# Kernel optimization log

Hardware: AMD Instinct MI355X
Metric: run time of the kernel (lower is better)

Reference implementation:

```python
import jax, jax.numpy as jnp
import numpy as np

B, T, N, H, P = 16, 64, 512, 128, 12


def _laplacian_with_self_loop(adj):
    a = adj + jnp.eye(adj.shape[0], dtype=adj.dtype)
    d_inv_sqrt = 1.0 / jnp.sqrt(a.sum(axis=1))
    return a * d_inv_sqrt[:, None] * d_inv_sqrt[None, :]


def setup_inputs() -> dict:
    key = jax.random.key(0)
    ks = jax.random.split(key, 10)
    inputs = jax.random.normal(ks[0], (B, T, N), dtype=jnp.float32)
    adj = jax.random.uniform(ks[1], (N, N), dtype=jnp.float32)
    adj = (adj + adj.T) * 0.5
    laplacian = _laplacian_with_self_loop(adj)

    def xavier(k, shape):
        fan_in, fan_out = shape[0], shape[1]
        lim = np.sqrt(6.0 / (fan_in + fan_out))
        return jax.random.uniform(k, shape, jnp.float32, -lim, lim)

    W1 = xavier(ks[2], (H + 1, 2 * H))      # graph_conv1 weights
    b1 = jnp.ones((2 * H,), jnp.float32)    # bias init 1.0
    W2 = xavier(ks[3], (H + 1, H))          # graph_conv2 weights
    b2 = jnp.zeros((H,), jnp.float32)
    att_w1 = xavier(ks[4], (H, 1))
    att_w2 = xavier(ks[5], (N, 1))
    att_w3 = xavier(ks[6], (N, 1))
    att_b1 = jnp.zeros((1,), jnp.float32)
    att_b2 = jnp.zeros((1,), jnp.float32)
    att_b3 = jnp.zeros((1,), jnp.float32)
    W_out = xavier(ks[7], (T, P))
    b_out = jnp.zeros((P,), jnp.float32)
    return dict(inputs=inputs, laplacian=laplacian, W1=W1, b1=b1, W2=W2, b2=b2,
                att_w1=att_w1, att_w2=att_w2, att_w3=att_w3,
                att_b1=att_b1, att_b2=att_b2, att_b3=att_b3,
                W_out=W_out, b_out=b_out)


def reference(inputs, laplacian, W1, b1, W2, b2,
              att_w1, att_w2, att_w3, att_b1, att_b2, att_b3,
              W_out, b_out):
    Bs, Ts, Ns = inputs.shape
    Hs = W2.shape[1]

    def graph_conv(x_t, h_flat, W, b):
        # x_t: [B,N]; h_flat: [B, N*H]
        h = h_flat.reshape(Bs, Ns, Hs)
        conc = jnp.concatenate([x_t[..., None], h], axis=-1)     # [B,N,H+1]
        agg = jnp.einsum('mn,bnc->bmc', laplacian, conc)          # [B,N,H+1]
        out = agg @ W + b                                         # [B,N,O]
        return out.reshape(Bs, -1)                                # [B,N*O] (flattened, matching torch)

    def step(h_flat, x_t):
        ru = jax.nn.sigmoid(graph_conv(x_t, h_flat, W1, b1))      # [B, N*2H]
        r, u = jnp.split(ru, 2, axis=1)                            # split on flattened dim (faithful)
        c = jnp.tanh(graph_conv(x_t, r * h_flat, W2, b2))          # [B, N*H]
        new_h = u * h_flat + (1.0 - u) * c
        return new_h, new_h

    h0 = jnp.zeros((Bs, Ns * Hs), inputs.dtype)
    _, hs = jax.lax.scan(step, h0, jnp.moveaxis(inputs, 1, 0))     # [T,B,N*H]
    hidden_states = jnp.moveaxis(hs, 0, 1).reshape(Bs, Ts, Ns, Hs)

    # SelfAttention: project H->1, then N->1 per (b,t), softmax over T
    hs1 = hidden_states.reshape(-1, Hs) @ att_w1 + att_b1          # [B*T*N, 1]
    f = (hs1.reshape(-1, Ns) @ att_w2 + att_b2).reshape(Bs, Ts)
    g = (hs1.reshape(-1, Ns) @ att_w3 + att_b3).reshape(Bs, Ts)
    beta = jax.nn.softmax(g * f, axis=-1)                          # [B,T]
    context = beta[:, :, None] * hs1.reshape(Bs, Ts, Ns)           # [B,T,N]

    context = context.transpose(0, 2, 1)                           # [B,N,T]
    Ps = W_out.shape[1]
    out = (context.reshape(-1, Ts) @ W_out + b_out).reshape(Bs, Ns, Ps)
    return out.transpose(0, 2, 1)                                  # [B,pre_len,N]
```

## Files before the change

kernel.cpp:

```cpp
#include <hip/hip_runtime.h>
#include <math.h>

#define B_ 16
#define T_ 64
#define N_ 512
#define H_ 128
#define P_ 12
#define NH 65536

__global__ __launch_bounds__(512) void lx_kernel(const float* __restrict__ x,
                                                 const float* __restrict__ L,
                                                 float* __restrict__ Lx) {
    __shared__ __align__(16) float xs[4][N_];
    const int r0 = blockIdx.x * 4;
    const int tid = threadIdx.x;
    for (int j = 0; j < 4; ++j)
        xs[j][tid] = x[(size_t)(r0 + j) * N_ + tid];
    __syncthreads();
    float a0 = 0.f, a1 = 0.f, a2 = 0.f, a3 = 0.f;
    const int m = tid;
#pragma unroll 8
    for (int n = 0; n < N_; ++n) {
        float lv = L[(size_t)n * N_ + m];
        a0 += xs[0][n] * lv;
        a1 += xs[1][n] * lv;
        a2 += xs[2][n] * lv;
        a3 += xs[3][n] * lv;
    }
    Lx[(size_t)(r0 + 0) * N_ + m] = a0;
    Lx[(size_t)(r0 + 1) * N_ + m] = a1;
    Lx[(size_t)(r0 + 2) * N_ + m] = a2;
    Lx[(size_t)(r0 + 3) * N_ + m] = a3;
}

__global__ __launch_bounds__(512) void gc1_kernel(
    const float* __restrict__ L, const float* __restrict__ Hprev,
    const float* __restrict__ Lx, const float* __restrict__ W1,
    const float* __restrict__ b1, float* __restrict__ rh,
    float* __restrict__ u, int t) {
    union Sm {
        struct { float Ht[2][64][128]; float Lt[2][64][33]; } p;
        float Wt[32][260];
    };
    __shared__ __align__(16) Sm sm;
    __shared__ __align__(16) float Zs[4][32][128];

    const int tid = threadIdx.x;
    const int b = blockIdx.x & 15;
    const int m0 = (blockIdx.x >> 4) * 32;
    const int g = tid >> 7;
    const int gt = tid & 127;
    const int tx = gt & 31, ty = gt >> 5;
    const int c0 = tx * 4;

    const float* __restrict__ Hb = Hprev + (size_t)b * NH;

    const int hrow = tid >> 5, hcol = (tid & 31) * 4;
    const int lm = tid >> 4, lk0 = (tid & 15) * 4;

    {
#pragma unroll
        for (int jj = 0; jj < 4; ++jj)
            *(float4*)&sm.p.Ht[0][hrow + 16 * jj][hcol] =
                *(const float4*)&Hb[(size_t)(hrow + 16 * jj) * H_ + hcol];
        float4 lv = *(const float4*)&L[(size_t)(m0 + lm) * N_ + lk0];
        sm.p.Lt[0][lk0 + 0][lm] = lv.x;
        sm.p.Lt[0][lk0 + 1][lm] = lv.y;
        sm.p.Lt[0][lk0 + 2][lm] = lv.z;
        sm.p.Lt[0][lk0 + 3][lm] = lv.w;
    }
    __syncthreads();

    float acc[8][4] = {};

    for (int kc = 0; kc < 8; ++kc) {
        const int bi = kc & 1, bj = bi ^ 1;
        float4 h0, h1, h2, h3, lv;
        if (kc < 7) {
            const size_t kb2 = (size_t)(kc + 1) * 64;
            h0 = *(const float4*)&Hb[(kb2 + hrow) * H_ + hcol];
            h1 = *(const float4*)&Hb[(kb2 + hrow + 16) * H_ + hcol];
            h2 = *(const float4*)&Hb[(kb2 + hrow + 32) * H_ + hcol];
            h3 = *(const float4*)&Hb[(kb2 + hrow + 48) * H_ + hcol];
            lv = *(const float4*)&L[(size_t)(m0 + lm) * N_ + kb2 + lk0];
        }
#pragma unroll
        for (int kk = 0; kk < 16; ++kk) {
            const int k = g * 16 + kk;
            const float4 la = *(const float4*)&sm.p.Lt[bi][k][ty * 8];
            const float4 lb = *(const float4*)&sm.p.Lt[bi][k][ty * 8 + 4];
            const float4 hv = *(const float4*)&sm.p.Ht[bi][k][c0];
#define FMA_ROW(r, s)                                                   \
            acc[r][0] += (s) * hv.x; acc[r][1] += (s) * hv.y;           \
            acc[r][2] += (s) * hv.z; acc[r][3] += (s) * hv.w;
            FMA_ROW(0, la.x) FMA_ROW(1, la.y) FMA_ROW(2, la.z) FMA_ROW(3, la.w)
            FMA_ROW(4, lb.x) FMA_ROW(5, lb.y) FMA_ROW(6, lb.z) FMA_ROW(7, lb.w)
#undef FMA_ROW
        }
        if (kc < 7) {
            *(float4*)&sm.p.Ht[bj][hrow][hcol] = h0;
            *(float4*)&sm.p.Ht[bj][hrow + 16][hcol] = h1;
            *(float4*)&sm.p.Ht[bj][hrow + 32][hcol] = h2;
            *(float4*)&sm.p.Ht[bj][hrow + 48][hcol] = h3;
            sm.p.Lt[bj][lk0 + 0][lm] = lv.x;
            sm.p.Lt[bj][lk0 + 1][lm] = lv.y;
            sm.p.Lt[bj][lk0 + 2][lm] = lv.z;
            sm.p.Lt[bj][lk0 + 3][lm] = lv.w;
        }
        __syncthreads();
    }

#pragma unroll
    for (int r = 0; r < 8; ++r)
        *(float4*)&Zs[g][ty * 8 + r][c0] =
            make_float4(acc[r][0], acc[r][1], acc[r][2], acc[r][3]);
    __syncthreads();

    for (int j = tid; j < 1024; j += 512) {
        const int m = j >> 5, cc = (j & 31) * 4;
        float4 z0 = *(const float4*)&Zs[0][m][cc];
        float4 z1 = *(const float4*)&Zs[1][m][cc];
        float4 z2 = *(const float4*)&Zs[2][m][cc];
        float4 z3 = *(const float4*)&Zs[3][m][cc];
        *(float4*)&Zs[0][m][cc] = make_float4(z0.x + z1.x + z2.x + z3.x,
                                              z0.y + z1.y + z2.y + z3.y,
                                              z0.z + z1.z + z2.z + z3.z,
                                              z0.w + z1.w + z2.w + z3.w);
    }
    __syncthreads();

    const int to = tid & 63, tm = tid >> 6;
    const int o0 = to * 4;
    float a2[4][4] = {};
    const int wr = tid >> 4, wc = (tid & 15) * 16;

    for (int c4 = 0; c4 < 4; ++c4) {
#pragma unroll
        for (int jj = 0; jj < 4; ++jj)
            *(float4*)&sm.Wt[wr][wc + 4 * jj] =
                *(const float4*)&W1[(size_t)(1 + c4 * 32 + wr) * 256 + wc + 4 * jj];
        __syncthreads();
#pragma unroll
        for (int ch4 = 0; ch4 < 8; ++ch4) {
            const float4 w0v = *(const float4*)&sm.Wt[ch4 * 4 + 0][o0];
            const float4 w1v = *(const float4*)&sm.Wt[ch4 * 4 + 1][o0];
            const float4 w2v = *(const float4*)&sm.Wt[ch4 * 4 + 2][o0];
            const float4 w3v = *(const float4*)&sm.Wt[ch4 * 4 + 3][o0];
#pragma unroll
            for (int i = 0; i < 4; ++i) {
                const float4 zv = *(const float4*)&Zs[0][tm + 8 * i][c4 * 32 + ch4 * 4];
                a2[i][0] += zv.x * w0v.x + zv.y * w1v.x + zv.z * w2v.x + zv.w * w3v.x;
                a2[i][1] += zv.x * w0v.y + zv.y * w1v.y + zv.z * w2v.y + zv.w * w3v.y;
                a2[i][2] += zv.x * w0v.z + zv.y * w1v.z + zv.z * w2v.z + zv.w * w3v.z;
                a2[i][3] += zv.x * w0v.w + zv.y * w1v.w + zv.z * w2v.w + zv.w * w3v.w;
            }
        }
        __syncthreads();
    }

    const float4 w0r = *(const float4*)&W1[o0];
    const float4 bbv = *(const float4*)&b1[o0];
    const float* __restrict__ LxRow = Lx + ((size_t)b * T_ + t) * N_ + m0;
    float* __restrict__ rhB = rh + (size_t)b * NH;
    float* __restrict__ uB = u + (size_t)b * NH;
    const bool isR = (m0 < 256);
#pragma unroll
    for (int i = 0; i < 4; ++i) {
        const int mi = tm + 8 * i;
        const float lx = LxRow[mi];
        float v0 = a2[i][0] + lx * w0r.x + bbv.x;
        float v1 = a2[i][1] + lx * w0r.y + bbv.y;
        float v2 = a2[i][2] + lx * w0r.z + bbv.z;
        float v3 = a2[i][3] + lx * w0r.w + bbv.w;
        float s0 = 1.f / (1.f + expf(-v0));
        float s1 = 1.f / (1.f + expf(-v1));
        float s2 = 1.f / (1.f + expf(-v2));
        float s3 = 1.f / (1.f + expf(-v3));
        const int fl = (m0 + mi) * 256 + o0;
        if (isR) {
            float4 hv = *(const float4*)&Hb[fl];
            *(float4*)&rhB[fl] = make_float4(s0 * hv.x, s1 * hv.y, s2 * hv.z, s3 * hv.w);
        } else {
            *(float4*)&uB[fl - NH] = make_float4(s0, s1, s2, s3);
        }
    }
}

__global__ __launch_bounds__(512) void gc2_kernel(
    const float* __restrict__ L, const float* __restrict__ Hprev,
    const float* __restrict__ rh, const float* __restrict__ u,
    const float* __restrict__ Lx, const float* __restrict__ W2,
    const float* __restrict__ b2, const float* __restrict__ aw1,
    const float* __restrict__ ab1, float* __restrict__ Hnew,
    float* __restrict__ hs1, int t) {
    union Sm {
        struct { float Ht[2][64][128]; float Lt[2][64][33]; } p;
        float Wt[32][132];
    };
    __shared__ __align__(16) Sm sm;
    __shared__ __align__(16) float Zs[4][32][128];
    __shared__ __align__(16) float red[32][32];

    const int tid = threadIdx.x;
    const int b = blockIdx.x & 15;
    const int m0 = (blockIdx.x >> 4) * 32;
    const int g = tid >> 7;
    const int gt = tid & 127;
    const int tx = gt & 31, ty = gt >> 5;
    const int c0 = tx * 4;

    const float* __restrict__ Rb = rh + (size_t)b * NH;
    const float* __restrict__ Hb = Hprev + (size_t)b * NH;
    const float* __restrict__ Ub = u + (size_t)b * NH;

    const int hrow = tid >> 5, hcol = (tid & 31) * 4;
    const int lm = tid >> 4, lk0 = (tid & 15) * 4;

    {
#pragma unroll
        for (int jj = 0; jj < 4; ++jj)
            *(float4*)&sm.p.Ht[0][hrow + 16 * jj][hcol] =
                *(const float4*)&Rb[(size_t)(hrow + 16 * jj) * H_ + hcol];
        float4 lv = *(const float4*)&L[(size_t)(m0 + lm) * N_ + lk0];
        sm.p.Lt[0][lk0 + 0][lm] = lv.x;
        sm.p.Lt[0][lk0 + 1][lm] = lv.y;
        sm.p.Lt[0][lk0 + 2][lm] = lv.z;
        sm.p.Lt[0][lk0 + 3][lm] = lv.w;
    }
    __syncthreads();

    float acc[8][4] = {};

    for (int kc = 0; kc < 8; ++kc) {
        const int bi = kc & 1, bj = bi ^ 1;
        float4 h0, h1, h2, h3, lv;
        if (kc < 7) {
            const size_t kb2 = (size_t)(kc + 1) * 64;
            h0 = *(const float4*)&Rb[(kb2 + hrow) * H_ + hcol];
            h1 = *(const float4*)&Rb[(kb2 + hrow + 16) * H_ + hcol];
            h2 = *(const float4*)&Rb[(kb2 + hrow + 32) * H_ + hcol];
            h3 = *(const float4*)&Rb[(kb2 + hrow + 48) * H_ + hcol];
            lv = *(const float4*)&L[(size_t)(m0 + lm) * N_ + kb2 + lk0];
        }
#pragma unroll
        for (int kk = 0; kk < 16; ++kk) {
            const int k = g * 16 + kk;
            const float4 la = *(const float4*)&sm.p.Lt[bi][k][ty * 8];
            const float4 lb = *(const float4*)&sm.p.Lt[bi][k][ty * 8 + 4];
            const float4 hv = *(const float4*)&sm.p.Ht[bi][k][c0];
#define FMA_ROW(r, s)                                                   \
            acc[r][0] += (s) * hv.x; acc[r][1] += (s) * hv.y;           \
            acc[r][2] += (s) * hv.z; acc[r][3] += (s) * hv.w;
            FMA_ROW(0, la.x) FMA_ROW(1, la.y) FMA_ROW(2, la.z) FMA_ROW(3, la.w)
            FMA_ROW(4, lb.x) FMA_ROW(5, lb.y) FMA_ROW(6, lb.z) FMA_ROW(7, lb.w)
#undef FMA_ROW
        }
        if (kc < 7) {
            *(float4*)&sm.p.Ht[bj][hrow][hcol] = h0;
            *(float4*)&sm.p.Ht[bj][hrow + 16][hcol] = h1;
            *(float4*)&sm.p.Ht[bj][hrow + 32][hcol] = h2;
            *(float4*)&sm.p.Ht[bj][hrow + 48][hcol] = h3;
            sm.p.Lt[bj][lk0 + 0][lm] = lv.x;
            sm.p.Lt[bj][lk0 + 1][lm] = lv.y;
            sm.p.Lt[bj][lk0 + 2][lm] = lv.z;
            sm.p.Lt[bj][lk0 + 3][lm] = lv.w;
        }
        __syncthreads();
    }

#pragma unroll
    for (int r = 0; r < 8; ++r)
        *(float4*)&Zs[g][ty * 8 + r][c0] =
            make_float4(acc[r][0], acc[r][1], acc[r][2], acc[r][3]);
    __syncthreads();

    for (int j = tid; j < 1024; j += 512) {
        const int m = j >> 5, cc = (j & 31) * 4;
        float4 z0 = *(const float4*)&Zs[0][m][cc];
        float4 z1 = *(const float4*)&Zs[1][m][cc];
        float4 z2 = *(const float4*)&Zs[2][m][cc];
        float4 z3 = *(const float4*)&Zs[3][m][cc];
        *(float4*)&Zs[0][m][cc] = make_float4(z0.x + z1.x + z2.x + z3.x,
                                              z0.y + z1.y + z2.y + z3.y,
                                              z0.z + z1.z + z2.z + z3.z,
                                              z0.w + z1.w + z2.w + z3.w);
    }
    __syncthreads();

    const int to = tid & 31, tm = tid >> 5;
    const int o0 = to * 4;
    float a2[2][4] = {};
    const int wr = tid >> 4, wc = (tid & 15) * 8;

    for (int c4 = 0; c4 < 4; ++c4) {
#pragma unroll
        for (int jj = 0; jj < 2; ++jj)
            *(float4*)&sm.Wt[wr][wc + 4 * jj] =
                *(const float4*)&W2[(size_t)(1 + c4 * 32 + wr) * H_ + wc + 4 * jj];
        __syncthreads();
#pragma unroll
        for (int ch4 = 0; ch4 < 8; ++ch4) {
            const float4 w0v = *(const float4*)&sm.Wt[ch4 * 4 + 0][o0];
            const float4 w1v = *(const float4*)&sm.Wt[ch4 * 4 + 1][o0];
            const float4 w2v = *(const float4*)&sm.Wt[ch4 * 4 + 2][o0];
            const float4 w3v = *(const float4*)&sm.Wt[ch4 * 4 + 3][o0];
#pragma unroll
            for (int i = 0; i < 2; ++i) {
                const float4 zv = *(const float4*)&Zs[0][tm + 16 * i][c4 * 32 + ch4 * 4];
                a2[i][0] += zv.x * w0v.x + zv.y * w1v.x + zv.z * w2v.x + zv.w * w3v.x;
                a2[i][1] += zv.x * w0v.y + zv.y * w1v.y + zv.z * w2v.y + zv.w * w3v.y;
                a2[i][2] += zv.x * w0v.z + zv.y * w1v.z + zv.z * w2v.z + zv.w * w3v.z;
                a2[i][3] += zv.x * w0v.w + zv.y * w1v.w + zv.z * w2v.w + zv.w * w3v.w;
            }
        }
        __syncthreads();
    }

    const float4 w0r = *(const float4*)&W2[o0];
    const float4 bbv = *(const float4*)&b2[o0];
    const float4 awv = *(const float4*)&aw1[o0];
    const float* __restrict__ LxRow = Lx + ((size_t)b * T_ + t) * N_ + m0;
    float* __restrict__ HnB = Hnew + (size_t)b * NH;
#pragma unroll
    for (int i = 0; i < 2; ++i) {
        const int mi = tm + 16 * i;
        const float lx = LxRow[mi];
        float c0e = tanhf(a2[i][0] + lx * w0r.x + bbv.x);
        float c1e = tanhf(a2[i][1] + lx * w0r.y + bbv.y);
        float c2e = tanhf(a2[i][2] + lx * w0r.z + bbv.z);
        float c3e = tanhf(a2[i][3] + lx * w0r.w + bbv.w);
        const int fl = (m0 + mi) * H_ + o0;
        float4 uv = *(const float4*)&Ub[fl];
        float4 hp = *(const float4*)&Hb[fl];
        float h0 = uv.x * hp.x + (1.f - uv.x) * c0e;
        float h1 = uv.y * hp.y + (1.f - uv.y) * c1e;
        float h2 = uv.z * hp.z + (1.f - uv.z) * c2e;
        float h3 = uv.w * hp.w + (1.f - uv.w) * c3e;
        *(float4*)&HnB[fl] = make_float4(h0, h1, h2, h3);
        red[mi][to] = h0 * awv.x + h1 * awv.y + h2 * awv.z + h3 * awv.w;
    }
    __syncthreads();
    if (tid < 32) {
        float s = 0.f;
#pragma unroll
        for (int k2 = 0; k2 < 32; ++k2) s += red[tid][k2];
        hs1[((size_t)b * T_ + t) * N_ + m0 + tid] = s + ab1[0];
    }
}

__global__ __launch_bounds__(64) void att_beta_kernel(
    const float* __restrict__ hs1, const float* __restrict__ aw2,
    const float* __restrict__ aw3, const float* __restrict__ ab2,
    const float* __restrict__ ab3, float* __restrict__ beta) {
    const int b = blockIdx.x;
    const int t = threadIdx.x;
    const float* __restrict__ row = hs1 + ((size_t)b * T_ + t) * N_;
    float f = 0.f, g = 0.f;
    for (int n = 0; n < N_; n += 4) {
        float4 hv = *(const float4*)&row[n];
        float4 w2v = *(const float4*)&aw2[n];
        float4 w3v = *(const float4*)&aw3[n];
        f += hv.x * w2v.x + hv.y * w2v.y + hv.z * w2v.z + hv.w * w2v.w;
        g += hv.x * w3v.x + hv.y * w3v.y + hv.z * w3v.z + hv.w * w3v.w;
    }
    f += ab2[0];
    g += ab3[0];
    float s = f * g;
    float mx = s;
    for (int off = 32; off; off >>= 1) mx = fmaxf(mx, __shfl_xor(mx, off));
    float e = expf(s - mx);
    float sum = e;
    for (int off = 32; off; off >>= 1) sum += __shfl_xor(sum, off);
    beta[b * T_ + t] = e / sum;
}

__global__ __launch_bounds__(256) void att_out_kernel(
    const float* __restrict__ hs1, const float* __restrict__ beta,
    const float* __restrict__ Wout, const float* __restrict__ bout,
    float* __restrict__ out) {
    __shared__ float bs[T_];
    __shared__ float ws[T_][P_];
    const int b = blockIdx.x;
    const int tid = threadIdx.x;
    if (tid < T_) bs[tid] = beta[b * T_ + tid];
    for (int i = tid; i < T_ * P_; i += 256) ws[i / P_][i % P_] = Wout[i];
    __syncthreads();
    for (int nn = 0; nn < 2; ++nn) {
        const int n = tid + nn * 256;
        float acc[P_];
#pragma unroll
        for (int p = 0; p < P_; ++p) acc[p] = bout[p];
        for (int t = 0; t < T_; ++t) {
            float v = bs[t] * hs1[((size_t)b * T_ + t) * N_ + n];
#pragma unroll
            for (int p = 0; p < P_; ++p) acc[p] += v * ws[t][p];
        }
#pragma unroll
        for (int p = 0; p < P_; ++p) out[((size_t)b * P_ + p) * N_ + n] = acc[p];
    }
}

extern "C" void kernel_launch(void* const* d_in, const int* in_sizes, int n_in,
                              void* d_out, int out_size, void* d_ws, size_t ws_size,
                              hipStream_t stream) {
    const float* x = (const float*)d_in[0];
    const float* L = (const float*)d_in[1];
    const float* W1 = (const float*)d_in[2];
    const float* b1 = (const float*)d_in[3];
    const float* W2 = (const float*)d_in[4];
    const float* b2 = (const float*)d_in[5];
    const float* aw1 = (const float*)d_in[6];
    const float* aw2 = (const float*)d_in[7];
    const float* aw3 = (const float*)d_in[8];
    const float* ab1 = (const float*)d_in[9];
    const float* ab2 = (const float*)d_in[10];
    const float* ab3 = (const float*)d_in[11];
    const float* Wout = (const float*)d_in[12];
    const float* bout = (const float*)d_in[13];
    float* out = (float*)d_out;

    float* ws = (float*)d_ws;
    float* Lx = ws;
    float* hs1 = Lx + B_ * T_ * N_;
    float* hb0 = hs1 + B_ * T_ * N_;
    float* hb1 = hb0 + (size_t)B_ * NH;
    float* rh = hb1 + (size_t)B_ * NH;
    float* u = rh + (size_t)B_ * NH;
    float* beta = u + (size_t)B_ * NH;
    (void)in_sizes; (void)n_in; (void)out_size; (void)ws_size;

    hipMemsetAsync(hb0, 0, (size_t)B_ * NH * sizeof(float), stream);
    lx_kernel<<<256, 512, 0, stream>>>(x, L, Lx);

    for (int t = 0; t < T_; ++t) {
        float* hp = (t & 1) ? hb1 : hb0;
        float* hn = (t & 1) ? hb0 : hb1;
        gc1_kernel<<<256, 512, 0, stream>>>(L, hp, Lx, W1, b1, rh, u, t);
        gc2_kernel<<<256, 512, 0, stream>>>(L, hp, rh, u, Lx, W2, b2, aw1, ab1,
                                            hn, hs1, t);
    }
    att_beta_kernel<<<16, 64, 0, stream>>>(hs1, aw2, aw3, ab2, ab3, beta);
    att_out_kernel<<<16, 256, 0, stream>>>(hs1, beta, Wout, bout, out);
}
```

Measured before the change: 4.448 ms.

## Shrink graph-conv tiles and shared memory to raise occupancy

Both GRU graph-conv kernels move from 64-wide K chunks with 4-way split-K and 8x4 register tiles to 32-wide K chunks with 2-way split-K and 4x4 register tiles. The weight staging buffer is halved to 16 rows. Together this cuts shared memory (no 4x Zs reduction buffer) and per-thread registers, so more blocks can sit on each CU. The cost is twice as many barrier-separated iterations and less arithmetic per shared-memory load.

Measured after the change: 4.008 ms. 9.9% less time.

```diff
diff --git a/kernel.cpp b/kernel.cpp
--- a/kernel.cpp
+++ b/kernel.cpp
@@ -38,117 +38,110 @@
     const float* __restrict__ Lx, const float* __restrict__ W1,
     const float* __restrict__ b1, float* __restrict__ rh,
     float* __restrict__ u, int t) {
-    union Sm {
-        struct { float Ht[2][64][128]; float Lt[2][64][33]; } p;
-        float Wt[32][260];
+    __shared__ __align__(16) float Ht[2][32][H_];
+    union LW {
+        float Lt[2][32][33];
+        float Wt[16][260];
     };
-    __shared__ __align__(16) Sm sm;
-    __shared__ __align__(16) float Zs[4][32][128];
+    __shared__ __align__(16) LW sm;
+    __shared__ __align__(16) float Zb[32][H_];
 
     const int tid = threadIdx.x;
     const int b = blockIdx.x & 15;
     const int m0 = (blockIdx.x >> 4) * 32;
-    const int g = tid >> 7;
-    const int gt = tid & 127;
+    const float* __restrict__ Hb = Hprev + (size_t)b * NH;
+
+    const int hrow = tid >> 5, hcol = (tid & 31) * 4;
+    const int lm = tid >> 4, lk0 = (tid & 15) * 2;
+
+    {
+        *(float4*)&Ht[0][hrow][hcol] = *(const float4*)&Hb[(size_t)hrow * H_ + hcol];
+        *(float4*)&Ht[0][hrow + 16][hcol] =
+            *(const float4*)&Hb[(size_t)(hrow + 16) * H_ + hcol];
+        float2 lv = *(const float2*)&L[(size_t)(m0 + lm) * N_ + lk0];
+        sm.Lt[0][lk0 + 0][lm] = lv.x;
+        sm.Lt[0][lk0 + 1][lm] = lv.y;
+    }
+    __syncthreads();
+
+    const int g = tid >> 8;
+    const int gt = tid & 255;
     const int tx = gt & 31, ty = gt >> 5;
-    const int c0 = tx * 4;
-
-    const float* __restrict__ Hb = Hprev + (size_t)b * NH;
-
-    const int hrow = tid >> 5, hcol = (tid & 31) * 4;
-    const int lm = tid >> 4, lk0 = (tid & 15) * 4;
-
-    {
-#pragma unroll
-        for (int jj = 0; jj < 4; ++jj)
-            *(float4*)&sm.p.Ht[0][hrow + 16 * jj][hcol] =
-                *(const float4*)&Hb[(size_t)(hrow + 16 * jj) * H_ + hcol];
-        float4 lv = *(const float4*)&L[(size_t)(m0 + lm) * N_ + lk0];
-        sm.p.Lt[0][lk0 + 0][lm] = lv.x;
-        sm.p.Lt[0][lk0 + 1][lm] = lv.y;
-        sm.p.Lt[0][lk0 + 2][lm] = lv.z;
-        sm.p.Lt[0][lk0 + 3][lm] = lv.w;
-    }
-    __syncthreads();
-
-    float acc[8][4] = {};
-
-    for (int kc = 0; kc < 8; ++kc) {
+    const int c0 = tx * 4, mrow = ty * 4;
+
+    float acc[4][4] = {};
+
+    for (int kc = 0; kc < 16; ++kc) {
         const int bi = kc & 1, bj = bi ^ 1;
-        float4 h0, h1, h2, h3, lv;
-        if (kc < 7) {
-            const size_t kb2 = (size_t)(kc + 1) * 64;
-            h0 = *(const float4*)&Hb[(kb2 + hrow) * H_ + hcol];
-            h1 = *(const float4*)&Hb[(kb2 + hrow + 16) * H_ + hcol];
-            h2 = *(const float4*)&Hb[(kb2 + hrow + 32) * H_ + hcol];
-            h3 = *(const float4*)&Hb[(kb2 + hrow + 48) * H_ + hcol];
-            lv = *(const float4*)&L[(size_t)(m0 + lm) * N_ + kb2 + lk0];
+        float4 p0, p1;
+        float2 pl;
+        if (kc < 15) {
+            const size_t kb = (size_t)(kc + 1) * 32;
+            p0 = *(const float4*)&Hb[(kb + hrow) * H_ + hcol];
+            p1 = *(const float4*)&Hb[(kb + hrow + 16) * H_ + hcol];
+            pl = *(const float2*)&L[(size_t)(m0 + lm) * N_ + kb + lk0];
         }
 #pragma unroll
         for (int kk = 0; kk < 16; ++kk) {
             const int k = g * 16 + kk;
-            const float4 la = *(const float4*)&sm.p.Lt[bi][k][ty * 8];
-            const float4 lb = *(const float4*)&sm.p.Lt[bi][k][ty * 8 + 4];
-            const float4 hv = *(const float4*)&sm.p.Ht[bi][k][c0];
-#define FMA_ROW(r, s)                                                   \
-            acc[r][0] += (s) * hv.x; acc[r][1] += (s) * hv.y;           \
-            acc[r][2] += (s) * hv.z; acc[r][3] += (s) * hv.w;
-            FMA_ROW(0, la.x) FMA_ROW(1, la.y) FMA_ROW(2, la.z) FMA_ROW(3, la.w)
-            FMA_ROW(4, lb.x) FMA_ROW(5, lb.y) FMA_ROW(6, lb.z) FMA_ROW(7, lb.w)
-#undef FMA_ROW
-        }
-        if (kc < 7) {
-            *(float4*)&sm.p.Ht[bj][hrow][hcol] = h0;
-            *(float4*)&sm.p.Ht[bj][hrow + 16][hcol] = h1;
-            *(float4*)&sm.p.Ht[bj][hrow + 32][hcol] = h2;
-            *(float4*)&sm.p.Ht[bj][hrow + 48][hcol] = h3;
-            sm.p.Lt[bj][lk0 + 0][lm] = lv.x;
-            sm.p.Lt[bj][lk0 + 1][lm] = lv.y;
-            sm.p.Lt[bj][lk0 + 2][lm] = lv.z;
-            sm.p.Lt[bj][lk0 + 3][lm] = lv.w;
-        }
-        __syncthreads();
-    }
-
-#pragma unroll
-    for (int r = 0; r < 8; ++r)
-        *(float4*)&Zs[g][ty * 8 + r][c0] =
-            make_float4(acc[r][0], acc[r][1], acc[r][2], acc[r][3]);
-    __syncthreads();
-
-    for (int j = tid; j < 1024; j += 512) {
-        const int m = j >> 5, cc = (j & 31) * 4;
-        float4 z0 = *(const float4*)&Zs[0][m][cc];
-        float4 z1 = *(const float4*)&Zs[1][m][cc];
-        float4 z2 = *(const float4*)&Zs[2][m][cc];
-        float4 z3 = *(const float4*)&Zs[3][m][cc];
-        *(float4*)&Zs[0][m][cc] = make_float4(z0.x + z1.x + z2.x + z3.x,
-                                              z0.y + z1.y + z2.y + z3.y,
-                                              z0.z + z1.z + z2.z + z3.z,
-                                              z0.w + z1.w + z2.w + z3.w);
+            const float4 la = *(const float4*)&sm.Lt[bi][k][mrow];
+            const float4 hv = *(const float4*)&Ht[bi][k][c0];
+            acc[0][0] += la.x * hv.x; acc[0][1] += la.x * hv.y;
+            acc[0][2] += la.x * hv.z; acc[0][3] += la.x * hv.w;
+            acc[1][0] += la.y * hv.x; acc[1][1] += la.y * hv.y;
+            acc[1][2] += la.y * hv.z; acc[1][3] += la.y * hv.w;
+            acc[2][0] += la.z * hv.x; acc[2][1] += la.z * hv.y;
+            acc[2][2] += la.z * hv.z; acc[2][3] += la.z * hv.w;
+            acc[3][0] += la.w * hv.x; acc[3][1] += la.w * hv.y;
+            acc[3][2] += la.w * hv.z; acc[3][3] += la.w * hv.w;
+        }
+        if (kc < 15) {
+            *(float4*)&Ht[bj][hrow][hcol] = p0;
+            *(float4*)&Ht[bj][hrow + 16][hcol] = p1;
+            sm.Lt[bj][lk0 + 0][lm] = pl.x;
+            sm.Lt[bj][lk0 + 1][lm] = pl.y;
+        }
+        __syncthreads();
+    }
+
+    if (g == 1) {
+#pragma unroll
+        for (int i = 0; i < 4; ++i)
+            *(float4*)&Zb[mrow + i][c0] =
+                make_float4(acc[i][0], acc[i][1], acc[i][2], acc[i][3]);
+    }
+    __syncthreads();
+    if (g == 0) {
+#pragma unroll
+        for (int i = 0; i < 4; ++i) {
+            float4 z = *(const float4*)&Zb[mrow + i][c0];
+            *(float4*)&Zb[mrow + i][c0] = make_float4(
+                acc[i][0] + z.x, acc[i][1] + z.y, acc[i][2] + z.z, acc[i][3] + z.w);
+        }
     }
     __syncthreads();
 
     const int to = tid & 63, tm = tid >> 6;
     const int o0 = to * 4;
     float a2[4][4] = {};
-    const int wr = tid >> 4, wc = (tid & 15) * 16;
-
-    for (int c4 = 0; c4 < 4; ++c4) {
-#pragma unroll
-        for (int jj = 0; jj < 4; ++jj)
-            *(float4*)&sm.Wt[wr][wc + 4 * jj] =
-                *(const float4*)&W1[(size_t)(1 + c4 * 32 + wr) * 256 + wc + 4 * jj];
-        __syncthreads();
-#pragma unroll
-        for (int ch4 = 0; ch4 < 8; ++ch4) {
+    const int wr = tid >> 5, wc = (tid & 31) * 4;
+
+    for (int ck = 0; ck < 8; ++ck) {
+        *(float4*)&sm.Wt[wr][wc] =
+            *(const float4*)&W1[(size_t)(1 + ck * 16 + wr) * 256 + wc];
+        *(float4*)&sm.Wt[wr][wc + 128] =
+            *(const float4*)&W1[(size_t)(1 + ck * 16 + wr) * 256 + wc + 128];
+        __syncthreads();
+#pragma unroll
+        for (int ch4 = 0; ch4 < 4; ++ch4) {
             const float4 w0v = *(const float4*)&sm.Wt[ch4 * 4 + 0][o0];
             const float4 w1v = *(const float4*)&sm.Wt[ch4 * 4 + 1][o0];
             const float4 w2v = *(const float4*)&sm.Wt[ch4 * 4 + 2][o0];
             const float4 w3v = *(const float4*)&sm.Wt[ch4 * 4 + 3][o0];
+            const int cc = ck * 16 + ch4 * 4;
 #pragma unroll
             for (int i = 0; i < 4; ++i) {
-                const float4 zv = *(const float4*)&Zs[0][tm + 8 * i][c4 * 32 + ch4 * 4];
+                const float4 zv = *(const float4*)&Zb[tm + 8 * i][cc];
                 a2[i][0] += zv.x * w0v.x + zv.y * w1v.x + zv.z * w2v.x + zv.w * w3v.x;
                 a2[i][1] += zv.x * w0v.y + zv.y * w1v.y + zv.z * w2v.y + zv.w * w3v.y;
                 a2[i][2] += zv.x * w0v.z + zv.y * w1v.z + zv.z * w2v.z + zv.w * w3v.z;
@@ -193,120 +186,111 @@
     const float* __restrict__ b2, const float* __restrict__ aw1,
     const float* __restrict__ ab1, float* __restrict__ Hnew,
     float* __restrict__ hs1, int t) {
-    union Sm {
-        struct { float Ht[2][64][128]; float Lt[2][64][33]; } p;
-        float Wt[32][132];
+    __shared__ __align__(16) float Ht[2][32][H_];
+    union LW {
+        float Lt[2][32][33];
+        float Wt[16][132];
     };
-    __shared__ __align__(16) Sm sm;
-    __shared__ __align__(16) float Zs[4][32][128];
+    __shared__ __align__(16) LW sm;
+    __shared__ __align__(16) float Zb[32][H_];
     __shared__ __align__(16) float red[32][32];
 
     const int tid = threadIdx.x;
     const int b = blockIdx.x & 15;
     const int m0 = (blockIdx.x >> 4) * 32;
-    const int g = tid >> 7;
-    const int gt = tid & 127;
-    const int tx = gt & 31, ty = gt >> 5;
-    const int c0 = tx * 4;
-
     const float* __restrict__ Rb = rh + (size_t)b * NH;
     const float* __restrict__ Hb = Hprev + (size_t)b * NH;
     const float* __restrict__ Ub = u + (size_t)b * NH;
 
     const int hrow = tid >> 5, hcol = (tid & 31) * 4;
-    const int lm = tid >> 4, lk0 = (tid & 15) * 4;
+    const int lm = tid >> 4, lk0 = (tid & 15) * 2;
 
     {
-#pragma unroll
-        for (int jj = 0; jj < 4; ++jj)
-            *(float4*)&sm.p.Ht[0][hrow + 16 * jj][hcol] =
-                *(const float4*)&Rb[(size_t)(hrow + 16 * jj) * H_ + hcol];
-        float4 lv = *(const float4*)&L[(size_t)(m0 + lm) * N_ + lk0];
-        sm.p.Lt[0][lk0 + 0][lm] = lv.x;
-        sm.p.Lt[0][lk0 + 1][lm] = lv.y;
-        sm.p.Lt[0][lk0 + 2][lm] = lv.z;
-        sm.p.Lt[0][lk0 + 3][lm] = lv.w;
-    }
-    __syncthreads();
-
-    float acc[8][4] = {};
-
-    for (int kc = 0; kc < 8; ++kc) {
+        *(float4*)&Ht[0][hrow][hcol] = *(const float4*)&Rb[(size_t)hrow * H_ + hcol];
+        *(float4*)&Ht[0][hrow + 16][hcol] =
+            *(const float4*)&Rb[(size_t)(hrow + 16) * H_ + hcol];
+        float2 lv = *(const float2*)&L[(size_t)(m0 + lm) * N_ + lk0];
+        sm.Lt[0][lk0 + 0][lm] = lv.x;
+        sm.Lt[0][lk0 + 1][lm] = lv.y;
+    }
+    __syncthreads();
+
+    const int g = tid >> 8;
+    const int gt = tid & 255;
+    const int tx = gt & 31, ty = gt >> 5;
+    const int c0 = tx * 4, mrow = ty * 4;
+
+    float acc[4][4] = {};
+
+    for (int kc = 0; kc < 16; ++kc) {
         const int bi = kc & 1, bj = bi ^ 1;
-        float4 h0, h1, h2, h3, lv;
-        if (kc < 7) {
-            const size_t kb2 = (size_t)(kc + 1) * 64;
-            h0 = *(const float4*)&Rb[(kb2 + hrow) * H_ + hcol];
-            h1 = *(const float4*)&Rb[(kb2 + hrow + 16) * H_ + hcol];
-            h2 = *(const float4*)&Rb[(kb2 + hrow + 32) * H_ + hcol];
-            h3 = *(const float4*)&Rb[(kb2 + hrow + 48) * H_ + hcol];
-            lv = *(const float4*)&L[(size_t)(m0 + lm) * N_ + kb2 + lk0];
+        float4 p0, p1;
+        float2 pl;
+        if (kc < 15) {
+            const size_t kb = (size_t)(kc + 1) * 32;
+            p0 = *(const float4*)&Rb[(kb + hrow) * H_ + hcol];
+            p1 = *(const float4*)&Rb[(kb + hrow + 16) * H_ + hcol];
+            pl = *(const float2*)&L[(size_t)(m0 + lm) * N_ + kb + lk0];
         }
 #pragma unroll
         for (int kk = 0; kk < 16; ++kk) {
             const int k = g * 16 + kk;
-            const float4 la = *(const float4*)&sm.p.Lt[bi][k][ty * 8];
-            const float4 lb = *(const float4*)&sm.p.Lt[bi][k][ty * 8 + 4];
-            const float4 hv = *(const float4*)&sm.p.Ht[bi][k][c0];
-#define FMA_ROW(r, s)                                                   \
-            acc[r][0] += (s) * hv.x; acc[r][1] += (s) * hv.y;           \
-            acc[r][2] += (s) * hv.z; acc[r][3] += (s) * hv.w;
-            FMA_ROW(0, la.x) FMA_ROW(1, la.y) FMA_ROW(2, la.z) FMA_ROW(3, la.w)
-            FMA_ROW(4, lb.x) FMA_ROW(5, lb.y) FMA_ROW(6, lb.z) FMA_ROW(7, lb.w)
-#undef FMA_ROW
-        }
-        if (kc < 7) {
-            *(float4*)&sm.p.Ht[bj][hrow][hcol] = h0;
-            *(float4*)&sm.p.Ht[bj][hrow + 16][hcol] = h1;
-            *(float4*)&sm.p.Ht[bj][hrow + 32][hcol] = h2;
-            *(float4*)&sm.p.Ht[bj][hrow + 48][hcol] = h3;
-            sm.p.Lt[bj][lk0 + 0][lm] = lv.x;
-            sm.p.Lt[bj][lk0 + 1][lm] = lv.y;
-            sm.p.Lt[bj][lk0 + 2][lm] = lv.z;
-            sm.p.Lt[bj][lk0 + 3][lm] = lv.w;
-        }
-        __syncthreads();
-    }
-
-#pragma unroll
-    for (int r = 0; r < 8; ++r)
-        *(float4*)&Zs[g][ty * 8 + r][c0] =
-            make_float4(acc[r][0], acc[r][1], acc[r][2], acc[r][3]);
-    __syncthreads();
-
-    for (int j = tid; j < 1024; j += 512) {
-        const int m = j >> 5, cc = (j & 31) * 4;
-        float4 z0 = *(const float4*)&Zs[0][m][cc];
-        float4 z1 = *(const float4*)&Zs[1][m][cc];
-        float4 z2 = *(const float4*)&Zs[2][m][cc];
-        float4 z3 = *(const float4*)&Zs[3][m][cc];
-        *(float4*)&Zs[0][m][cc] = make_float4(z0.x + z1.x + z2.x + z3.x,
-                                              z0.y + z1.y + z2.y + z3.y,
-                                              z0.z + z1.z + z2.z + z3.z,
-                                              z0.w + z1.w + z2.w + z3.w);
+            const float4 la = *(const float4*)&sm.Lt[bi][k][mrow];
+            const float4 hv = *(const float4*)&Ht[bi][k][c0];
+            acc[0][0] += la.x * hv.x; acc[0][1] += la.x * hv.y;
+            acc[0][2] += la.x * hv.z; acc[0][3] += la.x * hv.w;
+            acc[1][0] += la.y * hv.x; acc[1][1] += la.y * hv.y;
+            acc[1][2] += la.y * hv.z; acc[1][3] += la.y * hv.w;
+            acc[2][0] += la.z * hv.x; acc[2][1] += la.z * hv.y;
+            acc[2][2] += la.z * hv.z; acc[2][3] += la.z * hv.w;
+            acc[3][0] += la.w * hv.x; acc[3][1] += la.w * hv.y;
+            acc[3][2] += la.w * hv.z; acc[3][3] += la.w * hv.w;
+        }
+        if (kc < 15) {
+            *(float4*)&Ht[bj][hrow][hcol] = p0;
+            *(float4*)&Ht[bj][hrow + 16][hcol] = p1;
+            sm.Lt[bj][lk0 + 0][lm] = pl.x;
+            sm.Lt[bj][lk0 + 1][lm] = pl.y;
+        }
+        __syncthreads();
+    }
+
+    if (g == 1) {
+#pragma unroll
+        for (int i = 0; i < 4; ++i)
+            *(float4*)&Zb[mrow + i][c0] =
+                make_float4(acc[i][0], acc[i][1], acc[i][2], acc[i][3]);
+    }
+    __syncthreads();
+    if (g == 0) {
+#pragma unroll
+        for (int i = 0; i < 4; ++i) {
+            float4 z = *(const float4*)&Zb[mrow + i][c0];
+            *(float4*)&Zb[mrow + i][c0] = make_float4(
+                acc[i][0] + z.x, acc[i][1] + z.y, acc[i][2] + z.z, acc[i][3] + z.w);
+        }
     }
     __syncthreads();
 
     const int to = tid & 31, tm = tid >> 5;
     const int o0 = to * 4;
     float a2[2][4] = {};
-    const int wr = tid >> 4, wc = (tid & 15) * 8;
-
-    for (int c4 = 0; c4 < 4; ++c4) {
-#pragma unroll
-        for (int jj = 0; jj < 2; ++jj)
-            *(float4*)&sm.Wt[wr][wc + 4 * jj] =
-                *(const float4*)&W2[(size_t)(1 + c4 * 32 + wr) * H_ + wc + 4 * jj];
-        __syncthreads();
-#pragma unroll
-        for (int ch4 = 0; ch4 < 8; ++ch4) {
+    const int wr = tid >> 5, wc = (tid & 31) * 4;
+
+    for (int ck = 0; ck < 8; ++ck) {
+        *(float4*)&sm.Wt[wr][wc] =
+            *(const float4*)&W2[(size_t)(1 + ck * 16 + wr) * H_ + wc];
+        __syncthreads();
+#pragma unroll
+        for (int ch4 = 0; ch4 < 4; ++ch4) {
             const float4 w0v = *(const float4*)&sm.Wt[ch4 * 4 + 0][o0];
             const float4 w1v = *(const float4*)&sm.Wt[ch4 * 4 + 1][o0];
             const float4 w2v = *(const float4*)&sm.Wt[ch4 * 4 + 2][o0];
             const float4 w3v = *(const float4*)&sm.Wt[ch4 * 4 + 3][o0];
+            const int cc = ck * 16 + ch4 * 4;
 #pragma unroll
             for (int i = 0; i < 2; ++i) {
-                const float4 zv = *(const float4*)&Zs[0][tm + 16 * i][c4 * 32 + ch4 * 4];
+                const float4 zv = *(const float4*)&Zb[tm + 16 * i][cc];
                 a2[i][0] += zv.x * w0v.x + zv.y * w1v.x + zv.z * w2v.x + zv.w * w3v.x;
                 a2[i][1] += zv.x * w0v.y + zv.y * w1v.y + zv.z * w2v.y + zv.w * w3v.y;
                 a2[i][2] += zv.x * w0v.z + zv.y * w1v.z + zv.z * w2v.z + zv.w * w3v.z;
```
